# Performance work log

Hardware: AMD Instinct MI355X
Metric: run time of the kernel (lower is better)

The kernel has to match this reference:

```python
import jax, jax.numpy as jnp
import numpy as np
from jax import lax

B, T, N, H = 512, 128, 500, 1024
LB, UB = 0.0, 0.1
REBAL_ITERS = 20  # fixed unroll of the data-dependent while loop (converges immediately here)


def setup_inputs() -> dict:
    key = jax.random.key(0)
    ks = jax.random.split(key, 16)
    sN = 1.0 / np.sqrt(N)
    sH = 1.0 / np.sqrt(H)
    inp = {
        'x': jax.random.normal(ks[0], (B, T, N), jnp.float32),
        # GRU layer 0 (input N -> H), PyTorch gate order [r, z, n]
        'w_ih0': jax.random.normal(ks[1], (3 * H, N), jnp.float32) * sN,
        'w_hh0': jax.random.normal(ks[2], (3 * H, H), jnp.float32) * sH,
        'b_ih0': jax.random.normal(ks[3], (3 * H,), jnp.float32) * sH,
        'b_hh0': jax.random.normal(ks[4], (3 * H,), jnp.float32) * sH,
        # GRU layer 1 (H -> H)
        'w_ih1': jax.random.normal(ks[5], (3 * H, H), jnp.float32) * sH,
        'w_hh1': jax.random.normal(ks[6], (3 * H, H), jnp.float32) * sH,
        'b_ih1': jax.random.normal(ks[7], (3 * H,), jnp.float32) * sH,
        'b_hh1': jax.random.normal(ks[8], (3 * H,), jnp.float32) * sH,
        # score MLP: Linear(H,H) -> LayerNorm(H) -> SiLU -> Linear(H,N)
        'w1': jax.random.normal(ks[9], (H, H), jnp.float32) * sH,
        'b1': jax.random.normal(ks[10], (H,), jnp.float32) * sH,
        'ln_g': jnp.ones((H,), jnp.float32),
        'ln_b': jnp.zeros((H,), jnp.float32),
        'w2': jax.random.normal(ks[11], (N, H), jnp.float32) * sH,
        'b2': jax.random.normal(ks[12], (N,), jnp.float32) * sH,
    }
    return inp


def _gru_layer(x, w_ih, w_hh, b_ih, b_hh):
    # x: [B, T, D] -> hidden sequence [B, T, H]
    h_dim = w_hh.shape[1]
    x_proj = jnp.einsum('btd,gd->btg', x, w_ih) + b_ih  # [B, T, 3H]

    def step(h, xp):
        gh = jnp.einsum('bh,gh->bg', h, w_hh) + b_hh
        xr, xz, xn = jnp.split(xp, 3, axis=-1)
        hr, hz, hn = jnp.split(gh, 3, axis=-1)
        r = jax.nn.sigmoid(xr + hr)
        z = jax.nn.sigmoid(xz + hz)
        n = jnp.tanh(xn + r * hn)
        h_new = (1.0 - z) * n + z * h
        return h_new, h_new

    h0 = jnp.zeros((x.shape[0], h_dim), x.dtype)
    _, hs = lax.scan(step, h0, jnp.swapaxes(x_proj, 0, 1))  # [T, B, H]
    return jnp.swapaxes(hs, 0, 1)


def _rebalance(w, lb, ub):
    # vectorized, fixed-iteration version of the per-sample while loop
    n = w.shape[-1]
    w = jnp.clip(w, lb, ub)

    def body(w, _):
        excess = jnp.sum(w, axis=-1, keepdims=True) - 1.0
        active = excess > 1e-6
        surplus = jnp.maximum(w - ub, 0.0)
        tot_sur = jnp.sum(surplus, axis=-1, keepdims=True)
        upd = jnp.where(tot_sur > 0,
                        w - surplus / jnp.maximum(tot_sur, 1e-12) * excess,
                        w - excess / n)
        upd = jnp.clip(upd, lb, ub)
        return jnp.where(active, upd, w), None

    w, _ = lax.scan(body, w, None, length=REBAL_ITERS)
    return w


def reference(x, w_ih0, w_hh0, b_ih0, b_hh0, w_ih1, w_hh1, b_ih1, b_hh1,
              w1, b1, ln_g, ln_b, w2, b2):
    out = _gru_layer(x, w_ih0, w_hh0, b_ih0, b_hh0)
    out = _gru_layer(out, w_ih1, w_hh1, b_ih1, b_hh1)
    h_t = out[:, -1, :]  # [B, H]

    # score MLP (dropout is identity in eval)
    z = h_t @ w1.T + b1
    mu = jnp.mean(z, axis=-1, keepdims=True)
    var = jnp.var(z, axis=-1, keepdims=True)
    z = (z - mu) / jnp.sqrt(var + 1e-5) * ln_g + ln_b
    z = z * jax.nn.sigmoid(z)  # SiLU
    scores = z @ w2.T + b2  # [B, N]

    # LONG_ONLY (default True): negative scores -> -inf before softmax
    scores = jnp.where(scores < 0, -jnp.inf, scores)
    weights = jax.nn.softmax(scores, axis=-1)
    return _rebalance(weights, LB, UB)
```

## Files before the change

kernel.cpp:

```cpp
#include <hip/hip_runtime.h>
#include <hip/hip_cooperative_groups.h>
#include <math.h>

#define BATCH 512
#define SEQ_T 128
#define NIN   500
#define HID   1024
#define G3    3072

typedef float f32x4 __attribute__((ext_vector_type(4)));
typedef _Float16 half8 __attribute__((ext_vector_type(8)));

__device__ __forceinline__ void split_h2(float v, unsigned short &h, unsigned short &l) {
    _Float16 hh = (_Float16)v;
    float hf = (float)hh;
    if (fabsf(hf) < 6.103515625e-5f) { hh = (_Float16)0.f; hf = 0.f; }
    _Float16 ll = (_Float16)((v - hf) * 4096.f);
    h = __builtin_bit_cast(unsigned short, hh);
    l = __builtin_bit_cast(unsigned short, ll);
}

__device__ __forceinline__ float h2f(unsigned short u) {
    return (float)__builtin_bit_cast(_Float16, u);
}

__device__ __forceinline__ void g2lds16(const void* g, void* l) {
    __builtin_amdgcn_global_load_lds(
        (const __attribute__((address_space(1))) void*)g,
        (__attribute__((address_space(3))) void*)l,
        16, 0, 0);
}

__global__ __launch_bounds__(512, 2) void gru_fused(
    unsigned short* __restrict__ pH, unsigned short* __restrict__ pL,
    int nslots, int mode, int tt0, int nsteps,
    const unsigned short* __restrict__ Wh, const unsigned short* __restrict__ Wl,
    const float* __restrict__ bhh,
    const float* __restrict__ gx)
{
    __shared__ __align__(16) unsigned short lds[2][2560 * 8];
    __shared__ float red[64][96];

    const int tid  = threadIdx.x;
    const int lane = tid & 63;
    const int wave = tid >> 6;
    const int ms = wave >> 2, ns = (wave >> 1) & 1, wk = wave & 1;
    const int q = lane >> 4, l16 = lane & 15;
    const int mt = blockIdx.x >> 5, ht = blockIdx.x & 31;
    const int bm = mt << 6, hbase = ht << 5;

    const unsigned short* wsrc[3];
    #pragma unroll
    for (int i = 0; i < 3; i++) {
        int u = tid + 512 * i;
        int pl = u / 768; int rem = u - pl * 768;
        int oct = rem / 96; int r96 = rem - oct * 96;
        int g = r96 >> 5, wr = r96 & 31;
        wsrc[i] = (pl ? Wl : Wh) + (long)((g << 10) + hbase + wr) * 1024 + oct * 8;
    }

    const int erow = tid >> 3;
    const int ecg  = (tid & 7) << 2;
    const float4 br4 = *(const float4*)&bhh[hbase + ecg];
    const float4 bz4 = *(const float4*)&bhh[1024 + hbase + ecg];
    const float4 bn4 = *(const float4*)&bhh[2048 + hbase + ecg];
    const float ks = 1.0f / 4096.0f;

    for (int ttl = 0; ttl < nsteps; ttl++) {
        const int step = tt0 + ttl;
        const int rs    = (mode == 0) ? ((step + nslots - 1) % nslots) : (step & 1);
        const int wslot = (mode == 0) ? (step % nslots) : ((step & 1) ^ 1);
        const unsigned short* srcH = pH + (size_t)rs * 524288;
        const unsigned short* srcL = pL + (size_t)rs * 524288;
        unsigned short* dstH = pH + (size_t)wslot * 524288;
        unsigned short* dstL = pL + (size_t)wslot * 524288;
        const float* gxt = gx + (size_t)ttl * (512 * 3072);

        const unsigned short* aH = srcH + (long)(bm + lane) * 1024 + wave * 8;
        const unsigned short* aL = srcL + (long)(bm + lane) * 1024 + wave * 8;

        auto stage = [&](int b, int s) {
            const long ko = (long)s * 64;
            g2lds16(aH + ko,      &lds[b][(0 * 512 + wave * 64) * 8]);
            g2lds16(aL + ko,      &lds[b][(1 * 512 + wave * 64) * 8]);
            g2lds16(wsrc[0] + ko, &lds[b][(2 * 512 + wave * 64) * 8]);
            g2lds16(wsrc[1] + ko, &lds[b][(3 * 512 + wave * 64) * 8]);
            g2lds16(wsrc[2] + ko, &lds[b][(4 * 512 + wave * 64) * 8]);
        };

        f32x4 acc1[6] = {};
        f32x4 acc2[6] = {};
        stage(0, 0);
        int buf = 0;
        for (int s = 0; s < 16; s++) {
            __syncthreads();
            if (s < 15) stage(buf ^ 1, s + 1);
            half8 ah[2], al[2], bh[3], bl[3];
            const int koq = wk * 4 + q;
            #pragma unroll
            for (int ti = 0; ti < 2; ti++) {
                int r = ms * 32 + ti * 16 + l16;
                ah[ti] = *(const half8*)&lds[buf][(koq * 64 + r) * 8];
                al[ti] = *(const half8*)&lds[buf][(512 + koq * 64 + r) * 8];
            }
            #pragma unroll
            for (int tj = 0; tj < 3; tj++) {
                int r = ns * 48 + tj * 16 + l16;
                bh[tj] = *(const half8*)&lds[buf][(1024 + koq * 96 + r) * 8];
                bl[tj] = *(const half8*)&lds[buf][(1792 + koq * 96 + r) * 8];
            }
            #pragma unroll
            for (int ti = 0; ti < 2; ti++)
            #pragma unroll
            for (int tj = 0; tj < 3; tj++) {
                int t = ti * 3 + tj;
                acc1[t] = __builtin_amdgcn_mfma_f32_16x16x32_f16(ah[ti], bh[tj], acc1[t], 0, 0, 0);
                acc2[t] = __builtin_amdgcn_mfma_f32_16x16x32_f16(ah[ti], bl[tj], acc2[t], 0, 0, 0);
                acc2[t] = __builtin_amdgcn_mfma_f32_16x16x32_f16(al[ti], bh[tj], acc2[t], 0, 0, 0);
            }
            buf ^= 1;
        }
        __syncthreads();
        if (wk == 1) {
            #pragma unroll
            for (int ti = 0; ti < 2; ti++)
            #pragma unroll
            for (int tj = 0; tj < 3; tj++) {
                f32x4 c = acc1[ti * 3 + tj] + acc2[ti * 3 + tj] * ks;
                #pragma unroll
                for (int rr = 0; rr < 4; rr++)
                    red[ms * 32 + ti * 16 + q * 4 + rr][ns * 48 + tj * 16 + l16] = c[rr];
            }
        }
        __syncthreads();
        if (wk == 0) {
            #pragma unroll
            for (int ti = 0; ti < 2; ti++)
            #pragma unroll
            for (int tj = 0; tj < 3; tj++) {
                f32x4 c = acc1[ti * 3 + tj] + acc2[ti * 3 + tj] * ks;
                #pragma unroll
                for (int rr = 0; rr < 4; rr++) {
                    int row = ms * 32 + ti * 16 + q * 4 + rr;
                    int col = ns * 48 + tj * 16 + l16;
                    red[row][col] += c[rr];
                }
            }
        }
        __syncthreads();
        {
            const int grow = bm + erow;
            float4 sr = *(float4*)&red[erow][ecg];
            float4 sz = *(float4*)&red[erow][32 + ecg];
            float4 sn = *(float4*)&red[erow][64 + ecg];
            const float* gp = gxt + (long)grow * 3072 + hbase + ecg;
            float4 xr = *(const float4*)gp;
            float4 xz = *(const float4*)(gp + 1024);
            float4 xn = *(const float4*)(gp + 2048);
            const long po = (long)grow * 1024 + hbase + ecg;
            ushort4 hh4 = *(const ushort4*)&srcH[po];
            ushort4 hl4 = *(const ushort4*)&srcL[po];
            ushort4 oh, ol;
#define GRUC(c) { \
            float hp = h2f(hh4.c) + h2f(hl4.c) * ks; \
            float r_ = 1.f / (1.f + expf(-(xr.c + sr.c + br4.c))); \
            float z_ = 1.f / (1.f + expf(-(xz.c + sz.c + bz4.c))); \
            float n_ = tanhf(xn.c + r_ * (sn.c + bn4.c)); \
            float o_ = (1.f - z_) * n_ + z_ * hp; \
            split_h2(o_, oh.c, ol.c); }
            GRUC(x) GRUC(y) GRUC(z) GRUC(w)
#undef GRUC
            *(ushort4*)&dstH[po] = oh;
            *(ushort4*)&dstL[po] = ol;
        }
        if (ttl + 1 < nsteps) {
            __threadfence();
            cooperative_groups::this_grid().sync();
            __threadfence();
        }
    }
}

__global__ __launch_bounds__(256, 2) void gemm_h2(
    const unsigned short* __restrict__ Ah, const unsigned short* __restrict__ Al,
    const unsigned short* __restrict__ Bh, const unsigned short* __restrict__ Bl,
    const float* __restrict__ bias, float* __restrict__ C,
    int M, int NN, int Kp, int nnb)
{
    __shared__ __align__(16) unsigned short lds[2][4][8][64][8];

    const int id  = blockIdx.x;
    const int nns = nnb >> 3;
    const int xcd = id & 7;
    const int j   = id >> 3;
    const int bn  = (xcd * nns + j % nns) << 6;
    const int bm  = (j / nns) << 6;

    const int tid  = threadIdx.x;
    const int lane = tid & 63;
    const int wave = tid >> 6;
    const int ws   = wave & 1;
    const int wk   = wave >> 1;
    const int q    = lane >> 4;
    const int l16  = lane & 15;

    const unsigned short* gplane = (wave == 0) ? Ah : (wave == 1) ? Al
                                 : (wave == 2) ? Bh : Bl;
    const unsigned short* gsrc = gplane + (long)(((wave < 2) ? bm : bn) + lane) * Kp;

    f32x4 acc1[2][4] = {};
    f32x4 acc2[2][4] = {};

    const int NS = Kp >> 6;

    #pragma unroll
    for (int jk = 0; jk < 8; jk++)
        g2lds16(gsrc + jk * 8, &lds[0][wave][jk][0][0]);

    int buf = 0;
    for (int s = 0; s < NS; s++) {
        __syncthreads();
        if (s + 1 < NS) {
            const unsigned short* g2 = gsrc + (s + 1) * 64;
            #pragma unroll
            for (int jk = 0; jk < 8; jk++)
                g2lds16(g2 + jk * 8, &lds[buf ^ 1][wave][jk][0][0]);
        }
        const int ko = wk * 4 + q;
        half8 ah[2], al[2], bh[4], bl[4];
        #pragma unroll
        for (int ti = 0; ti < 2; ti++) {
            ah[ti] = *(const half8*)&lds[buf][0][ko][ws * 32 + ti * 16 + l16][0];
            al[ti] = *(const half8*)&lds[buf][1][ko][ws * 32 + ti * 16 + l16][0];
        }
        #pragma unroll
        for (int tj = 0; tj < 4; tj++) {
            bh[tj] = *(const half8*)&lds[buf][2][ko][tj * 16 + l16][0];
            bl[tj] = *(const half8*)&lds[buf][3][ko][tj * 16 + l16][0];
        }
        #pragma unroll
        for (int ti = 0; ti < 2; ti++)
        #pragma unroll
        for (int tj = 0; tj < 4; tj++) {
            acc1[ti][tj] = __builtin_amdgcn_mfma_f32_16x16x32_f16(ah[ti], bh[tj], acc1[ti][tj], 0, 0, 0);
            acc2[ti][tj] = __builtin_amdgcn_mfma_f32_16x16x32_f16(ah[ti], bl[tj], acc2[ti][tj], 0, 0, 0);
            acc2[ti][tj] = __builtin_amdgcn_mfma_f32_16x16x32_f16(al[ti], bh[tj], acc2[ti][tj], 0, 0, 0);
        }
        buf ^= 1;
    }

    __syncthreads();
    float* red = (float*)&lds[0][0][0][0][0];
    const float kscale = 1.0f / 4096.0f;
    if (wk == 1) {
        #pragma unroll
        for (int ti = 0; ti < 2; ti++)
        #pragma unroll
        for (int tj = 0; tj < 4; tj++) {
            f32x4 c = acc1[ti][tj] + acc2[ti][tj] * kscale;
            #pragma unroll
            for (int r = 0; r < 4; r++)
                red[(ws * 32 + ti * 16 + q * 4 + r) * 64 + tj * 16 + l16] = c[r];
        }
    }
    __syncthreads();
    if (wk == 0) {
        #pragma unroll
        for (int ti = 0; ti < 2; ti++)
        #pragma unroll
        for (int tj = 0; tj < 4; tj++) {
            int gn = bn + tj * 16 + l16;
            if (gn < NN) {
                float bv = bias[gn];
                f32x4 c = acc1[ti][tj] + acc2[ti][tj] * kscale;
                #pragma unroll
                for (int r = 0; r < 4; r++) {
                    int row = ws * 32 + ti * 16 + q * 4 + r;
                    C[(long)(bm + row) * NN + gn] = c[r] + red[row * 64 + tj * 16 + l16] + bv;
                }
            }
        }
    }
}

__global__ __launch_bounds__(256) void split_mat(
    const float* __restrict__ src, long outer_stride, long inner_stride, int inner_shift,
    int R, int C, int cshift,
    unsigned short* __restrict__ ph, unsigned short* __restrict__ pl)
{
    int t = blockIdx.x * 256 + threadIdx.x;
    int row = t >> cshift;
    int c0 = (t & ((1 << cshift) - 1)) << 3;
    float v[8];
    if (row < R) {
        const float* s = src + ((long)(row >> inner_shift)) * outer_stride
                             + ((long)(row & ((1 << inner_shift) - 1))) * inner_stride;
        if (c0 + 8 <= C) {
            float4 a = *(const float4*)(s + c0);
            float4 b = *(const float4*)(s + c0 + 4);
            v[0]=a.x; v[1]=a.y; v[2]=a.z; v[3]=a.w;
            v[4]=b.x; v[5]=b.y; v[6]=b.z; v[7]=b.w;
        } else {
            #pragma unroll
            for (int j2 = 0; j2 < 8; j2++) { int cc = c0 + j2; v[j2] = (cc < C) ? s[cc] : 0.f; }
        }
    } else {
        #pragma unroll
        for (int j2 = 0; j2 < 8; j2++) v[j2] = 0.f;
    }
    unsigned short hh[8], ll[8];
    #pragma unroll
    for (int j2 = 0; j2 < 8; j2++) split_h2(v[j2], hh[j2], ll[j2]);
    long o = ((long)t << 3);
    ushort4 h0 = {hh[0],hh[1],hh[2],hh[3]}, h1 = {hh[4],hh[5],hh[6],hh[7]};
    ushort4 l0 = {ll[0],ll[1],ll[2],ll[3]}, l1 = {ll[4],ll[5],ll[6],ll[7]};
    *(ushort4*)&ph[o] = h0; *(ushort4*)&ph[o + 4] = h1;
    *(ushort4*)&pl[o] = l0; *(ushort4*)&pl[o + 4] = l1;
}

__device__ __forceinline__ float block_reduce_sum(float v) {
    __shared__ float red[4];
    #pragma unroll
    for (int o = 32; o > 0; o >>= 1) v += __shfl_down(v, o);
    __syncthreads();
    if ((threadIdx.x & 63) == 0) red[threadIdx.x >> 6] = v;
    __syncthreads();
    return red[0] + red[1] + red[2] + red[3];
}

__device__ __forceinline__ float block_reduce_max(float v) {
    __shared__ float red[4];
    #pragma unroll
    for (int o = 32; o > 0; o >>= 1) v = fmaxf(v, __shfl_down(v, o));
    __syncthreads();
    if ((threadIdx.x & 63) == 0) red[threadIdx.x >> 6] = v;
    __syncthreads();
    return fmaxf(fmaxf(red[0], red[1]), fmaxf(red[2], red[3]));
}

__global__ __launch_bounds__(256) void ln_silu(
    float* __restrict__ z,
    const float* __restrict__ gamma,
    const float* __restrict__ beta,
    unsigned short* __restrict__ ph, unsigned short* __restrict__ pl)
{
    int b = blockIdx.x;
    float* row = z + (long)b * HID;
    float v[4];
    float s = 0.f;
    #pragma unroll
    for (int i = 0; i < 4; i++) { v[i] = row[threadIdx.x + 256 * i]; s += v[i]; }
    float mean = block_reduce_sum(s) * (1.f / HID);
    float vs = 0.f;
    #pragma unroll
    for (int i = 0; i < 4; i++) { float d = v[i] - mean; vs += d * d; }
    float var = block_reduce_sum(vs) * (1.f / HID);
    float inv = 1.f / sqrtf(var + 1e-5f);
    #pragma unroll
    for (int i = 0; i < 4; i++) {
        int col = threadIdx.x + 256 * i;
        float zz = (v[i] - mean) * inv * gamma[col] + beta[col];
        float sv = zz / (1.f + expf(-zz));
        row[col] = sv;
        unsigned short hh, ll;
        split_h2(sv, hh, ll);
        ph[(long)b * HID + col] = hh;
        pl[(long)b * HID + col] = ll;
    }
}

__global__ __launch_bounds__(256) void head_softmax_rebalance(
    const float* __restrict__ scores,
    float* __restrict__ out)
{
    int b = blockIdx.x;
    const float* srow = scores + (long)b * NIN;
    int i0 = threadIdx.x;
    int i1 = threadIdx.x + 256;
    bool v1 = (i1 < NIN);

    float s0 = srow[i0];
    if (s0 < 0.f) s0 = -INFINITY;
    float s1 = v1 ? srow[i1] : -INFINITY;
    if (s1 < 0.f) s1 = -INFINITY;

    float m  = block_reduce_max(fmaxf(s0, s1));
    float e0 = expf(s0 - m);
    float e1 = v1 ? expf(s1 - m) : 0.f;
    float Z  = block_reduce_sum(e0 + e1);

    float w0 = fminf(fmaxf(e0 / Z, 0.f), 0.1f);
    float w1 = v1 ? fminf(fmaxf(e1 / Z, 0.f), 0.1f) : 0.f;

    for (int it = 0; it < 20; it++) {
        float total  = block_reduce_sum(w0 + w1);
        float excess = total - 1.f;
        bool active  = excess > 1e-6f;
        float sur0 = fmaxf(w0 - 0.1f, 0.f);
        float sur1 = fmaxf(w1 - 0.1f, 0.f);
        float totsur = block_reduce_sum(sur0 + sur1);
        float u0, u1;
        if (totsur > 0.f) {
            float k = excess / fmaxf(totsur, 1e-12f);
            u0 = w0 - sur0 * k;
            u1 = w1 - sur1 * k;
        } else {
            u0 = w0 - excess / (float)NIN;
            u1 = w1 - excess / (float)NIN;
        }
        u0 = fminf(fmaxf(u0, 0.f), 0.1f);
        u1 = fminf(fmaxf(u1, 0.f), 0.1f);
        if (active) { w0 = u0; w1 = u1; }
    }

    out[(long)b * NIN + i0] = w0;
    if (v1) out[(long)b * NIN + i1] = w1;
}

extern "C" void kernel_launch(void* const* d_in, const int* in_sizes, int n_in,
                              void* d_out, int out_size, void* d_ws, size_t ws_size,
                              hipStream_t stream)
{
    const float* x     = (const float*)d_in[0];
    const float* w_ih0 = (const float*)d_in[1];
    const float* w_hh0 = (const float*)d_in[2];
    const float* b_ih0 = (const float*)d_in[3];
    const float* b_hh0 = (const float*)d_in[4];
    const float* w_ih1 = (const float*)d_in[5];
    const float* w_hh1 = (const float*)d_in[6];
    const float* b_ih1 = (const float*)d_in[7];
    const float* b_hh1 = (const float*)d_in[8];
    const float* w1    = (const float*)d_in[9];
    const float* b1    = (const float*)d_in[10];
    const float* ln_g  = (const float*)d_in[11];
    const float* ln_b  = (const float*)d_in[12];
    const float* w2    = (const float*)d_in[13];
    const float* b2    = (const float*)d_in[14];
    float* out = (float*)d_out;

    static int use_coop = -1;
    if (use_coop < 0) {
        int dev = 0; hipGetDevice(&dev);
        int ca = 0;
        hipDeviceGetAttribute(&ca, hipDeviceAttributeCooperativeLaunch, dev);
        int nb = 0;
        hipError_t e = hipOccupancyMaxActiveBlocksPerMultiprocessor(&nb, gru_fused, 512, 0);
        use_coop = (ca && e == hipSuccess && nb >= 1) ? 1 : 0;
    }

    float* wsf = (float*)d_ws;
    auto alloc = [&](size_t nfl) { float* p = wsf; wsf += (nfl + 15) & ~(size_t)15; return p; };

    const size_t BH  = (size_t)BATCH * HID;
    const size_t BG  = (size_t)BATCH * G3;

    float* zb = alloc(BH);
    float* sc = alloc((size_t)BATCH * NIN);
    unsigned short* pzbh = (unsigned short*)alloc(BH / 2);
    unsigned short* pzbl = (unsigned short*)alloc(BH / 2);
    unsigned short* ph1  = (unsigned short*)alloc(BH);
    unsigned short* pl1  = (unsigned short*)alloc(BH);
    const size_t W0 = (size_t)G3 * 512;
    const size_t WH = (size_t)G3 * HID;
    const size_t W1s = (size_t)HID * HID;
    const size_t W2s = (size_t)512 * HID;
    unsigned short* pwih0h = (unsigned short*)alloc(W0 / 2);
    unsigned short* pwih0l = (unsigned short*)alloc(W0 / 2);
    unsigned short* pwhh0h = (unsigned short*)alloc(WH / 2);
    unsigned short* pwhh0l = (unsigned short*)alloc(WH / 2);
    unsigned short* pwih1h = (unsigned short*)alloc(WH / 2);
    unsigned short* pwih1l = (unsigned short*)alloc(WH / 2);
    unsigned short* pwhh1h = (unsigned short*)alloc(WH / 2);
    unsigned short* pwhh1l = (unsigned short*)alloc(WH / 2);
    unsigned short* pw1h   = (unsigned short*)alloc(W1s / 2);
    unsigned short* pw1l   = (unsigned short*)alloc(W1s / 2);
    unsigned short* pw2h   = (unsigned short*)alloc(W2s / 2);
    unsigned short* pw2l   = (unsigned short*)alloc(W2s / 2);
    size_t fixed_floats = (size_t)(wsf - (float*)d_ws);

    int Tc = 2;
    const int cands[7] = {128, 64, 32, 16, 8, 4, 2};
    for (int ci = 0; ci < 7; ci++) {
        size_t need = fixed_floats + (size_t)cands[ci] * 2359296ULL + 4096;
        if (need * sizeof(float) <= ws_size) { Tc = cands[ci]; break; }
    }
    float* gxc = alloc((size_t)Tc * BG);
    unsigned short* pxh = (unsigned short*)alloc((size_t)Tc * BATCH * 512 / 2);
    unsigned short* pxl = (unsigned short*)alloc((size_t)Tc * BATCH * 512 / 2);
    unsigned short* ph0 = (unsigned short*)alloc((size_t)Tc * BH / 2);
    unsigned short* pl0 = (unsigned short*)alloc((size_t)Tc * BH / 2);

    hipMemsetAsync(ph0 + (size_t)(Tc - 1) * BH, 0, BH * sizeof(unsigned short), stream);
    hipMemsetAsync(pl0 + (size_t)(Tc - 1) * BH, 0, BH * sizeof(unsigned short), stream);
    hipMemsetAsync(ph1, 0, BH * sizeof(unsigned short), stream);
    hipMemsetAsync(pl1, 0, BH * sizeof(unsigned short), stream);

    dim3 blk(256);

    split_mat<<<dim3(G3 * 512 / 2048), blk, 0, stream>>>(w_ih0, 0L, (long)NIN, 30, G3, NIN, 6, pwih0h, pwih0l);
    split_mat<<<dim3(G3 * HID / 2048), blk, 0, stream>>>(w_hh0, 0L, (long)HID, 30, G3, HID, 7, pwhh0h, pwhh0l);
    split_mat<<<dim3(G3 * HID / 2048), blk, 0, stream>>>(w_ih1, 0L, (long)HID, 30, G3, HID, 7, pwih1h, pwih1l);
    split_mat<<<dim3(G3 * HID / 2048), blk, 0, stream>>>(w_hh1, 0L, (long)HID, 30, G3, HID, 7, pwhh1h, pwhh1l);
    split_mat<<<dim3(HID * HID / 2048), blk, 0, stream>>>(w1, 0L, (long)HID, 30, HID, HID, 7, pw1h, pw1l);
    split_mat<<<dim3(512 * HID / 2048), blk, 0, stream>>>(w2, 0L, (long)HID, 30, NIN, HID, 7, pw2h, pw2l);

    auto launch_gru = [&](unsigned short* pHb, unsigned short* pLb, int nslots, int mode,
                          int tt0, int nsteps,
                          const unsigned short* Whp, const unsigned short* Wlp,
                          const float* bhhp, const float* gxp) {
        if (use_coop) {
            void* args[] = {&pHb, &pLb, &nslots, &mode, &tt0, &nsteps,
                            (void*)&Whp, (void*)&Wlp, (void*)&bhhp, (void*)&gxp};
            hipLaunchCooperativeKernel(gru_fused, dim3(256), dim3(512), args, 0, stream);
        } else {
            for (int tt = 0; tt < nsteps; tt++)
                gru_fused<<<dim3(256), dim3(512), 0, stream>>>(
                    pHb, pLb, nslots, mode, tt0 + tt, 1, Whp, Wlp, bhhp,
                    gxp + (size_t)tt * (512 * 3072));
        }
    };

    for (int c = 0; c < SEQ_T / Tc; c++) {
        int t0 = c * Tc;
        split_mat<<<dim3(Tc * BATCH * 512 / 2048), blk, 0, stream>>>(
            x + (long)t0 * NIN, (long)NIN, (long)SEQ_T * NIN, 9,
            Tc * BATCH, NIN, 6, pxh, pxl);
        gemm_h2<<<dim3((Tc * BATCH / 64) * 48), blk, 0, stream>>>(
            pxh, pxl, pwih0h, pwih0l, b_ih0, gxc, Tc * BATCH, G3, 512, 48);
        launch_gru(ph0, pl0, Tc, 0, 0, Tc, pwhh0h, pwhh0l, b_hh0, gxc);
        gemm_h2<<<dim3((Tc * BATCH / 64) * 48), blk, 0, stream>>>(
            ph0, pl0, pwih1h, pwih1l, b_ih1, gxc, Tc * BATCH, G3, 1024, 48);
        launch_gru(ph1, pl1, 2, 1, t0, Tc, pwhh1h, pwhh1l, b_hh1, gxc);
    }
    gemm_h2<<<dim3(8 * 16), blk, 0, stream>>>(ph1, pl1, pw1h, pw1l, b1, zb, BATCH, HID, 1024, 16);
    ln_silu<<<dim3(BATCH), blk, 0, stream>>>(zb, ln_g, ln_b, pzbh, pzbl);
    gemm_h2<<<dim3(8 * 8), blk, 0, stream>>>(pzbh, pzbl, pw2h, pw2l, b2, sc, BATCH, NIN, 1024, 8);
    head_softmax_rebalance<<<dim3(BATCH), blk, 0, stream>>>(sc, out);
}
```

Measured before the change: 13.93 ms.

## Replace cooperative grid sync with atomic barrier and triple-buffer GRU k-loop

Result: slower. 14.59 ms (+4.8%).

```diff
diff --git a/kernel.cpp b/kernel.cpp
--- a/kernel.cpp
+++ b/kernel.cpp
@@ -1,5 +1,4 @@
 #include <hip/hip_runtime.h>
-#include <hip/hip_cooperative_groups.h>
 #include <math.h>
 
 #define BATCH 512
@@ -31,14 +30,28 @@
         16, 0, 0);
 }
 
-__global__ __launch_bounds__(512, 2) void gru_fused(
+__device__ __forceinline__ void grid_barrier(unsigned* cnt, unsigned target) {
+    __syncthreads();
+    if (threadIdx.x == 0) {
+        __threadfence();
+        __hip_atomic_fetch_add(cnt, 1u, __ATOMIC_RELAXED, __HIP_MEMORY_SCOPE_AGENT);
+        while (__hip_atomic_load(cnt, __ATOMIC_RELAXED, __HIP_MEMORY_SCOPE_AGENT) < target)
+            __builtin_amdgcn_s_sleep(1);
+        __threadfence();
+    }
+    __syncthreads();
+    asm volatile("" ::: "memory");
+}
+
+__global__ __launch_bounds__(512, 1) void gru_fused(
     unsigned short* __restrict__ pH, unsigned short* __restrict__ pL,
     int nslots, int mode, int tt0, int nsteps,
     const unsigned short* __restrict__ Wh, const unsigned short* __restrict__ Wl,
     const float* __restrict__ bhh,
-    const float* __restrict__ gx)
+    const float* __restrict__ gx,
+    unsigned* bar)
 {
-    __shared__ __align__(16) unsigned short lds[2][2560 * 8];
+    __shared__ __align__(16) unsigned short lds[3][2560 * 8];
     __shared__ float red[64][96];
 
     const int tid  = threadIdx.x;
@@ -65,6 +78,8 @@
     const float4 bz4 = *(const float4*)&bhh[1024 + hbase + ecg];
     const float4 bn4 = *(const float4*)&bhh[2048 + hbase + ecg];
     const float ks = 1.0f / 4096.0f;
+    const int grow = bm + erow;
+    const long po = (long)grow * 1024 + hbase + ecg;
 
     for (int ttl = 0; ttl < nsteps; ttl++) {
         const int step = tt0 + ttl;
@@ -79,6 +94,13 @@
         const unsigned short* aH = srcH + (long)(bm + lane) * 1024 + wave * 8;
         const unsigned short* aL = srcL + (long)(bm + lane) * 1024 + wave * 8;
 
+        const float* gp = gxt + (long)grow * 3072 + hbase + ecg;
+        float4 xr = *(const float4*)gp;
+        float4 xz = *(const float4*)(gp + 1024);
+        float4 xn = *(const float4*)(gp + 2048);
+        ushort4 hh4 = *(const ushort4*)&srcH[po];
+        ushort4 hl4 = *(const ushort4*)&srcL[po];
+
         auto stage = [&](int b, int s) {
             const long ko = (long)s * 64;
             g2lds16(aH + ko,      &lds[b][(0 * 512 + wave * 64) * 8]);
@@ -91,23 +113,28 @@
         f32x4 acc1[6] = {};
         f32x4 acc2[6] = {};
         stage(0, 0);
-        int buf = 0;
+        stage(1, 1);
+        #pragma unroll
         for (int s = 0; s < 16; s++) {
-            __syncthreads();
-            if (s < 15) stage(buf ^ 1, s + 1);
+            if (s < 15)
+                asm volatile("s_waitcnt vmcnt(5) lgkmcnt(0)\n\ts_barrier" ::: "memory");
+            else
+                asm volatile("s_waitcnt vmcnt(0) lgkmcnt(0)\n\ts_barrier" ::: "memory");
+            if (s + 2 < 16) stage((s + 2) % 3, s + 2);
+            const int bsel = s % 3;
+            const int koq = wk * 4 + q;
             half8 ah[2], al[2], bh[3], bl[3];
-            const int koq = wk * 4 + q;
             #pragma unroll
             for (int ti = 0; ti < 2; ti++) {
                 int r = ms * 32 + ti * 16 + l16;
-                ah[ti] = *(const half8*)&lds[buf][(koq * 64 + r) * 8];
-                al[ti] = *(const half8*)&lds[buf][(512 + koq * 64 + r) * 8];
+                ah[ti] = *(const half8*)&lds[bsel][(koq * 64 + r) * 8];
+                al[ti] = *(const half8*)&lds[bsel][(512 + koq * 64 + r) * 8];
             }
             #pragma unroll
             for (int tj = 0; tj < 3; tj++) {
                 int r = ns * 48 + tj * 16 + l16;
-                bh[tj] = *(const half8*)&lds[buf][(1024 + koq * 96 + r) * 8];
-                bl[tj] = *(const half8*)&lds[buf][(1792 + koq * 96 + r) * 8];
+                bh[tj] = *(const half8*)&lds[bsel][(1024 + koq * 96 + r) * 8];
+                bl[tj] = *(const half8*)&lds[bsel][(1792 + koq * 96 + r) * 8];
             }
             #pragma unroll
             for (int ti = 0; ti < 2; ti++)
@@ -118,7 +145,6 @@
                 acc2[t] = __builtin_amdgcn_mfma_f32_16x16x32_f16(ah[ti], bl[tj], acc2[t], 0, 0, 0);
                 acc2[t] = __builtin_amdgcn_mfma_f32_16x16x32_f16(al[ti], bh[tj], acc2[t], 0, 0, 0);
             }
-            buf ^= 1;
         }
         __syncthreads();
         if (wk == 1) {
@@ -149,17 +175,9 @@
         }
         __syncthreads();
         {
-            const int grow = bm + erow;
             float4 sr = *(float4*)&red[erow][ecg];
             float4 sz = *(float4*)&red[erow][32 + ecg];
             float4 sn = *(float4*)&red[erow][64 + ecg];
-            const float* gp = gxt + (long)grow * 3072 + hbase + ecg;
-            float4 xr = *(const float4*)gp;
-            float4 xz = *(const float4*)(gp + 1024);
-            float4 xn = *(const float4*)(gp + 2048);
-            const long po = (long)grow * 1024 + hbase + ecg;
-            ushort4 hh4 = *(const ushort4*)&srcH[po];
-            ushort4 hl4 = *(const ushort4*)&srcL[po];
             ushort4 oh, ol;
 #define GRUC(c) { \
             float hp = h2f(hh4.c) + h2f(hl4.c) * ks; \
@@ -173,11 +191,8 @@
             *(ushort4*)&dstH[po] = oh;
             *(ushort4*)&dstL[po] = ol;
         }
-        if (ttl + 1 < nsteps) {
-            __threadfence();
-            cooperative_groups::this_grid().sync();
-            __threadfence();
-        }
+        if (ttl + 1 < nsteps)
+            grid_barrier(bar, 256u * (unsigned)(ttl + 1));
     }
 }
 
@@ -445,7 +460,9 @@
         hipDeviceGetAttribute(&ca, hipDeviceAttributeCooperativeLaunch, dev);
         int nb = 0;
         hipError_t e = hipOccupancyMaxActiveBlocksPerMultiprocessor(&nb, gru_fused, 512, 0);
-        use_coop = (ca && e == hipSuccess && nb >= 1) ? 1 : 0;
+        int ncu = 0;
+        hipDeviceGetAttribute(&ncu, hipDeviceAttributeMultiprocessorCount, dev);
+        use_coop = (ca && e == hipSuccess && nb >= 1 && ncu * nb >= 256) ? 1 : 0;
     }
 
     float* wsf = (float*)d_ws;
@@ -454,6 +471,7 @@
     const size_t BH  = (size_t)BATCH * HID;
     const size_t BG  = (size_t)BATCH * G3;
 
+    unsigned* bar = (unsigned*)alloc(16);
     float* zb = alloc(BH);
     float* sc = alloc((size_t)BATCH * NIN);
     unsigned short* pzbh = (unsigned short*)alloc(BH / 2);
@@ -509,14 +527,16 @@
                           const unsigned short* Whp, const unsigned short* Wlp,
                           const float* bhhp, const float* gxp) {
         if (use_coop) {
+            hipMemsetAsync(bar, 0, sizeof(unsigned), stream);
             void* args[] = {&pHb, &pLb, &nslots, &mode, &tt0, &nsteps,
-                            (void*)&Whp, (void*)&Wlp, (void*)&bhhp, (void*)&gxp};
+                            (void*)&Whp, (void*)&Wlp, (void*)&bhhp, (void*)&gxp,
+                            (void*)&bar};
             hipLaunchCooperativeKernel(gru_fused, dim3(256), dim3(512), args, 0, stream);
         } else {
             for (int tt = 0; tt < nsteps; tt++)
                 gru_fused<<<dim3(256), dim3(512), 0, stream>>>(
                     pHb, pLb, nslots, mode, tt0 + tt, 1, Whp, Wlp, bhhp,
-                    gxp + (size_t)tt * (512 * 3072));
+                    gxp + (size_t)tt * (512 * 3072), bar);
         }
     };
 
```
